# Performance work log

Hardware: AMD Instinct MI355X
Metric: run time of the kernel (lower is better)

## Reference

```python
import jax, jax.numpy as jnp
import numpy as np

H = 768   # hidden_size
E = 9     # num_entity_types
R = 10    # num_relation_types
B, S, N = 8, 4096, 64
P = N * (N - 1) // 2  # 2016 ordered pairs i<j


def setup_inputs() -> dict:
    key = jax.random.key(0)
    ks = jax.random.split(key, 10)
    sd = 0.02
    return {
        "sequence_output": jax.random.normal(ks[0], (B, S, H), jnp.float32),
        "attention_mask": jnp.ones((B, S), jnp.int32),
        "entity_spans": jnp.sort(jax.random.randint(ks[1], (B, N, 2), 0, S), axis=-1),
        # entity_classifier: Linear(H, H//2) -> ReLU -> Linear(H//2, E)
        "w1": jax.random.normal(ks[2], (H, H // 2), jnp.float32) * sd,
        "b1": jnp.zeros((H // 2,), jnp.float32),
        "w2": jax.random.normal(ks[3], (H // 2, E), jnp.float32) * sd,
        "b2": jnp.zeros((E,), jnp.float32),
        # relation_classifier: Linear(2H, H) -> ReLU -> Linear(H, R)
        "rw1": jax.random.normal(ks[4], (2 * H, H), jnp.float32) * sd,
        "rb1": jnp.zeros((H,), jnp.float32),
        "rw2": jax.random.normal(ks[5], (H, R), jnp.float32) * sd,
        "rb2": jnp.zeros((R,), jnp.float32),
    }


def reference(sequence_output, attention_mask, entity_spans,
              w1, b1, w2, b2, rw1, rb1, rw2, rb2):
    # entity classifier over all tokens (dropout is identity in eval)
    h = jax.nn.relu(jnp.einsum('bsh,hf->bsf', sequence_output, w1) + b1)
    entity_logits = jnp.einsum('bsf,fe->bse', h, w2) + b2  # [B,S,E]

    # span mean-pooling via a [B,N,S] membership mask (segment-mean)
    pos = jnp.arange(S)
    start = entity_spans[..., 0:1]  # [B,N,1]
    end = entity_spans[..., 1:2]    # [B,N,1]
    mask = ((pos >= start) & (pos < end)).astype(sequence_output.dtype)  # [B,N,S]
    counts = jnp.clip(mask.sum(-1, keepdims=True), 1.0)  # avoid /0 for empty spans
    entity_reprs = jnp.einsum('bns,bsh->bnh', mask, sequence_output) / counts  # [B,N,H]
    pooled_logits = jnp.einsum('bns,bse->bne', mask, entity_logits) / counts   # [B,N,E]
    entity_types = jnp.argmax(pooled_logits, axis=-1)  # [B,N]

    # all i<j pairs, batched relation classifier (replaces per-pair Python loop)
    ii, jj = np.triu_indices(N, k=1)  # static index sets, len P
    pair = jnp.concatenate([entity_reprs[:, ii], entity_reprs[:, jj]], axis=-1)  # [B,P,2H]
    rh = jax.nn.relu(jnp.einsum('bpk,kh->bph', pair, rw1) + rb1)
    relation_logits = jnp.einsum('bph,hr->bpr', rh, rw2) + rb2  # [B,P,R]
    relation_types = jnp.argmax(relation_logits, axis=-1)  # [B,P]

    return entity_logits, relation_logits, entity_reprs, entity_types, relation_types
```

## Files before the change

### kernel.cpp

```cpp
#include <hip/hip_runtime.h>
#include <hip/hip_bf16.h>

#define Hh 768
#define Ff 384
#define Ee 9
#define Rr 10
#define Bb 8
#define Ss 4096
#define Nn_ENT 64
#define Pp 2016
#define CH 16
#define NC 256

typedef short bf16x8 __attribute__((ext_vector_type(8)));
typedef float f32x4 __attribute__((ext_vector_type(4)));

__device__ __forceinline__ void async_copy16(void* lds, const void* g) {
  auto* l = (__attribute__((address_space(3))) unsigned int*)(lds);
  auto* p = (const __attribute__((address_space(1))) unsigned int*)(g);
  __builtin_amdgcn_global_load_lds(p, l, 16, 0, 0);
}

__global__ __launch_bounds__(256) void transpose_w1(const float* __restrict__ w1,
                                                    unsigned short* __restrict__ wt) {
  __shared__ unsigned short tile[64][65];
  const int bk = blockIdx.x * 64;
  const int bc = blockIdx.y * 64;
  const int c = threadIdx.x & 63, kq = threadIdx.x >> 6;
#pragma unroll
  for (int i = 0; i < 16; ++i) {
    int k = kq * 16 + i;
    float v = w1[(size_t)(bk + k) * Ff + bc + c];
    tile[c][k] = __bfloat16_as_ushort(__float2bfloat16(v));
  }
  __syncthreads();
  const int k2 = threadIdx.x & 63, cq = threadIdx.x >> 6;
#pragma unroll
  for (int i = 0; i < 16; ++i) {
    int c2 = cq * 16 + i;
    wt[(size_t)(bc + c2) * Hh + bk + k2] = tile[c2][k2];
  }
}

__global__ __launch_bounds__(512, 4) void gemm1_fused(const float* __restrict__ A,
                                                      const unsigned short* __restrict__ Wt,
                                                      const float* __restrict__ b1,
                                                      const float* __restrict__ w2,
                                                      const float* __restrict__ b2,
                                                      float* __restrict__ elog,
                                                      float* __restrict__ Pc) {
  __shared__ float As[64 * 64];
  __shared__ unsigned short Bs[384 * 64];
  __shared__ float w2s[Ff * Ee];
  __shared__ float b1s[Ff];
  __shared__ float b2s[Ee];
  float* red = (float*)&Bs[0];

  const int t = threadIdx.x;
  const int wid = t >> 6, lane = t & 63;
  const int wm = wid >> 2, wn = wid & 3;
  const int fr = lane & 15, fq = lane >> 4;
  const int row0 = blockIdx.x * 64;
  const int bb = row0 >> 12;
  const int c0 = (row0 & (Ss - 1)) >> 4;

  for (int i = t; i < Ff * Ee; i += 512) w2s[i] = w2[i];
  for (int i = t; i < Ff; i += 512) b1s[i] = b1[i];
  if (t < Ee) b2s[t] = b2[t];

  const int brow0 = (lane >> 3);
  const int bgr = lane & 7;

  f32x4 acc[2][6] = {};
  const int sB = (fr & 7);

#pragma unroll 1
  for (int ks = 0; ks < Hh / 64; ++ks) {
    const int k0 = ks * 64;
#pragma unroll
    for (int i = 0; i < 2; ++i) {
      const int rl = (wid * 2 + i) * 4 + (lane >> 4);
      const int g = (lane & 15) ^ (rl & 15);
      async_copy16(&As[(wid * 2 + i) * 256],
                   A + (size_t)(row0 + rl) * Hh + k0 + g * 4);
    }
#pragma unroll
    for (int j = 0; j < 6; ++j) {
      const int e = wid * 6 + j;
      const int rl = e * 8 + brow0;
      const int g = bgr ^ (rl & 7);
      async_copy16(&Bs[e * 512],
                   Wt + (size_t)rl * Hh + k0 + g * 8);
    }
    __syncthreads();

#pragma unroll
    for (int kk = 0; kk < 2; ++kk) {
      bf16x8 af[2], bfr[6];
#pragma unroll
      for (int m = 0; m < 2; ++m) {
        const int R = wm * 32 + m * 16 + fr;
        const int G0 = 2 * (kk * 4 + fq);
        const float* rowp = &As[R * 64];
        float4 v0 = *(const float4*)(rowp + ((G0 ^ fr) * 4));
        float4 v1 = *(const float4*)(rowp + (((G0 + 1) ^ fr) * 4));
        union { bf16x8 v; __hip_bfloat162 h2[4]; } u;
        u.h2[0] = __float22bfloat162_rn(float2{v0.x, v0.y});
        u.h2[1] = __float22bfloat162_rn(float2{v0.z, v0.w});
        u.h2[2] = __float22bfloat162_rn(float2{v1.x, v1.y});
        u.h2[3] = __float22bfloat162_rn(float2{v1.z, v1.w});
        af[m] = u.v;
      }
      const int gB = ((kk * 4 + fq) ^ sB) * 8;
#pragma unroll
      for (int n = 0; n < 6; ++n)
        bfr[n] = *(const bf16x8*)&Bs[(wn * 96 + n * 16 + fr) * 64 + gB];
#pragma unroll
      for (int m = 0; m < 2; ++m)
#pragma unroll
        for (int n = 0; n < 6; ++n)
          acc[m][n] = __builtin_amdgcn_mfma_f32_16x16x32_bf16(af[m], bfr[n], acc[m][n], 0, 0, 0);
    }

    if (t < 256) {
      const int cc = t >> 6, kq = lane & 15, rh = lane >> 4;
      float4 s = {0.f, 0.f, 0.f, 0.f};
#pragma unroll
      for (int q = 0; q < 4; ++q) {
        const int row = cc * 16 + rh * 4 + q;
        const int slot = kq ^ (rh * 4 + q);
        float4 v = *(const float4*)&As[row * 64 + slot * 4];
        s.x += v.x; s.y += v.y; s.z += v.z; s.w += v.w;
      }
      s.x += __shfl_xor(s.x, 16); s.y += __shfl_xor(s.y, 16);
      s.z += __shfl_xor(s.z, 16); s.w += __shfl_xor(s.w, 16);
      s.x += __shfl_xor(s.x, 32); s.y += __shfl_xor(s.y, 32);
      s.z += __shfl_xor(s.z, 32); s.w += __shfl_xor(s.w, 32);
      if (rh == 0)
        *(float4*)&Pc[((size_t)(bb * NC + c0 + cc)) * Hh + k0 + kq * 4] = s;
    }
    __syncthreads();
  }

#pragma unroll
  for (int m = 0; m < 2; ++m) {
#pragma unroll
    for (int j = 0; j < 4; ++j) {
      float p[Ee];
#pragma unroll
      for (int e = 0; e < Ee; ++e) p[e] = 0.f;
#pragma unroll
      for (int n = 0; n < 6; ++n) {
        const int col = wn * 96 + n * 16 + fr;
        const float hv = fmaxf(acc[m][n][j] + b1s[col], 0.f);
        const float* wrow = &w2s[col * Ee];
#pragma unroll
        for (int e = 0; e < Ee; ++e) p[e] = fmaf(hv, wrow[e], p[e]);
      }
#pragma unroll
      for (int mask = 1; mask <= 8; mask <<= 1)
#pragma unroll
        for (int e = 0; e < Ee; ++e) p[e] += __shfl_xor(p[e], mask);
      if (fr < Ee) {
        const int row = wm * 32 + m * 16 + fq * 4 + j;
        red[(wn * 64 + row) * Ee + fr] = p[fr];
      }
    }
  }
  __syncthreads();
  for (int idx = t; idx < 64 * Ee; idx += 512) {
    const int row = idx / Ee, e = idx - row * Ee;
    float v = red[(0 * 64 + row) * Ee + e] + red[(1 * 64 + row) * Ee + e]
            + red[(2 * 64 + row) * Ee + e] + red[(3 * 64 + row) * Ee + e] + b2s[e];
    elog[(size_t)(row0 + row) * Ee + e] = v;
  }
}

__global__ __launch_bounds__(256) void gemm_uv_splitk(const float* __restrict__ A,
                                                      const float* __restrict__ rw1,
                                                      float* __restrict__ part) {
  const int uv = blockIdx.z & 1, ks = blockIdx.z >> 1;
  const float* Wp = rw1 + (size_t)uv * Hh * Hh + (size_t)ks * 192 * Hh;
  __shared__ float Ast[16][68];
  __shared__ float Wst[16][68];
  const int t = threadIdx.x;
  const int row0 = blockIdx.x * 64, col0 = blockIdx.y * 64;
  const int tm = (t & 15) * 4, tn = (t >> 4) * 4;
  const int lr = t >> 2, lk = (t & 3) * 4;
  const int wk = t >> 4, wc = (t & 15) * 4;
  float acc[4][4] = {};
  const float* Arow = A + (size_t)(row0 + lr) * Hh + ks * 192 + lk;
  for (int k0 = 0; k0 < 192; k0 += 16) {
    float4 av = *(const float4*)(Arow + k0);
    Ast[lk + 0][lr] = av.x; Ast[lk + 1][lr] = av.y;
    Ast[lk + 2][lr] = av.z; Ast[lk + 3][lr] = av.w;
    *(float4*)&Wst[wk][wc] = *(const float4*)(Wp + (size_t)(k0 + wk) * Hh + col0 + wc);
    __syncthreads();
#pragma unroll
    for (int kk = 0; kk < 16; ++kk) {
      const float4 a = *(const float4*)&Ast[kk][tm];
      const float4 b = *(const float4*)&Wst[kk][tn];
      acc[0][0] = fmaf(a.x, b.x, acc[0][0]); acc[0][1] = fmaf(a.x, b.y, acc[0][1]);
      acc[0][2] = fmaf(a.x, b.z, acc[0][2]); acc[0][3] = fmaf(a.x, b.w, acc[0][3]);
      acc[1][0] = fmaf(a.y, b.x, acc[1][0]); acc[1][1] = fmaf(a.y, b.y, acc[1][1]);
      acc[1][2] = fmaf(a.y, b.z, acc[1][2]); acc[1][3] = fmaf(a.y, b.w, acc[1][3]);
      acc[2][0] = fmaf(a.z, b.x, acc[2][0]); acc[2][1] = fmaf(a.z, b.y, acc[2][1]);
      acc[2][2] = fmaf(a.z, b.z, acc[2][2]); acc[2][3] = fmaf(a.z, b.w, acc[2][3]);
      acc[3][0] = fmaf(a.w, b.x, acc[3][0]); acc[3][1] = fmaf(a.w, b.y, acc[3][1]);
      acc[3][2] = fmaf(a.w, b.z, acc[3][2]); acc[3][3] = fmaf(a.w, b.w, acc[3][3]);
    }
    __syncthreads();
  }
  float* out = part + ((size_t)ks * 2 + uv) * (512 * Hh);
#pragma unroll
  for (int i = 0; i < 4; ++i) {
    float4 o; o.x = acc[i][0]; o.y = acc[i][1]; o.z = acc[i][2]; o.w = acc[i][3];
    *(float4*)(out + (size_t)(row0 + tm + i) * Hh + col0 + tn) = o;
  }
}

__global__ __launch_bounds__(256) void uv_reduce(const float* __restrict__ part,
                                                 float* __restrict__ uv) {
  const int i = blockIdx.x * 256 + threadIdx.x;
  const float4* p = (const float4*)part;
  float4 a = p[i], b = p[i + 196608], c = p[i + 2 * 196608], d = p[i + 3 * 196608];
  float4 o;
  o.x = (a.x + b.x) + (c.x + d.x);
  o.y = (a.y + b.y) + (c.y + d.y);
  o.z = (a.z + b.z) + (c.z + d.z);
  o.w = (a.w + b.w) + (c.w + d.w);
  ((float4*)uv)[i] = o;
}

__global__ __launch_bounds__(256) void chunk_scan(float* __restrict__ Pc) {
  __shared__ float tile[NC][64];
  const int b = blockIdx.y;
  const int h0 = blockIdx.x * 64;
  float* base = Pc + (size_t)b * NC * Hh + h0;
  const int l = threadIdx.x & 63, g = threadIdx.x >> 6;
#pragma unroll 4
  for (int c = g * 64; c < g * 64 + 64; ++c)
    tile[c][l] = base[(size_t)c * Hh + l];
  __syncthreads();
  float run = 0.f;
#pragma unroll 4
  for (int c = g * 64; c < g * 64 + 64; ++c) {
    run += tile[c][l];
    tile[c][l] = run;
  }
  __syncthreads();
  float off = 0.f;
#pragma unroll
  for (int gg = 0; gg < 3; ++gg)
    if (gg < g) off += tile[gg * 64 + 63][l];
  __syncthreads();
  if (g > 0) {
#pragma unroll 4
    for (int c = g * 64; c < g * 64 + 64; ++c)
      tile[c][l] += off;
  }
  __syncthreads();
#pragma unroll 4
  for (int c = g * 64; c < g * 64 + 64; ++c)
    base[(size_t)c * Hh + l] = tile[c][l];
}

__global__ __launch_bounds__(192) void entity_reprs_k(const float* __restrict__ seq,
                                                      const float* __restrict__ Pc,
                                                      const int* __restrict__ spans,
                                                      float* __restrict__ reprs) {
  const int bn = blockIdx.x;
  const int b = bn >> 6;
  const int start = spans[bn * 2], end = spans[bn * 2 + 1];
  const int cnt = max(end - start, 1);
  const float inv = 1.0f / (float)cnt;
  const int cs = (start + CH - 1) >> 4, ce = end >> 4;
  const float* seqb = seq + (size_t)b * Ss * Hh;
  const float4* Pcb = (const float4*)(Pc + (size_t)b * NC * Hh);
  const int t = threadIdx.x;
  float4 acc = {0.f, 0.f, 0.f, 0.f};
  if (cs <= ce) {
    if (cs < ce) {
      float4 hi = Pcb[(size_t)(ce - 1) * 192 + t];
      acc.x += hi.x; acc.y += hi.y; acc.z += hi.z; acc.w += hi.w;
      if (cs > 0) {
        float4 lo = Pcb[(size_t)(cs - 1) * 192 + t];
        acc.x -= lo.x; acc.y -= lo.y; acc.z -= lo.z; acc.w -= lo.w;
      }
    }
    for (int s = start; s < cs * CH; ++s) {
      float4 v = ((const float4*)(seqb + (size_t)s * Hh))[t];
      acc.x += v.x; acc.y += v.y; acc.z += v.z; acc.w += v.w;
    }
    for (int s = ce * CH; s < end; ++s) {
      float4 v = ((const float4*)(seqb + (size_t)s * Hh))[t];
      acc.x += v.x; acc.y += v.y; acc.z += v.z; acc.w += v.w;
    }
  } else {
    for (int s = start; s < end; ++s) {
      float4 v = ((const float4*)(seqb + (size_t)s * Hh))[t];
      acc.x += v.x; acc.y += v.y; acc.z += v.z; acc.w += v.w;
    }
  }
  float4 o; o.x = acc.x * inv; o.y = acc.y * inv; o.z = acc.z * inv; o.w = acc.w * inv;
  ((float4*)(reprs + (size_t)bn * Hh))[t] = o;
}

__global__ __launch_bounds__(256) void pooled_argmax(const float* __restrict__ elog,
                                                     const int* __restrict__ spans,
                                                     float* __restrict__ etypes) {
  __shared__ float red[4][Ee];
  const int bn = blockIdx.x;
  const int b = bn >> 6;
  const int start = spans[bn * 2], end = spans[bn * 2 + 1];
  const int t = threadIdx.x, lane = t & 63, w = t >> 6;
  float acc[Ee];
#pragma unroll
  for (int e = 0; e < Ee; ++e) acc[e] = 0.f;
  const float* p = elog + (size_t)b * Ss * Ee;
  for (int s = start + t; s < end; s += 256) {
    const float* q = p + (size_t)s * Ee;
#pragma unroll
    for (int e = 0; e < Ee; ++e) acc[e] += q[e];
  }
#pragma unroll
  for (int off = 32; off; off >>= 1)
#pragma unroll
    for (int e = 0; e < Ee; ++e) acc[e] += __shfl_down(acc[e], off);
  if (lane == 0) {
#pragma unroll
    for (int e = 0; e < Ee; ++e) red[w][e] = acc[e];
  }
  __syncthreads();
  if (t == 0) {
    int best = 0; float bv = -1e30f;
#pragma unroll
    for (int e = 0; e < Ee; ++e) {
      float v = red[0][e] + red[1][e] + red[2][e] + red[3][e];
      if (v > bv) { bv = v; best = e; }
    }
    etypes[bn] = (float)best;
  }
}

__global__ __launch_bounds__(256) void relations_k(const float* __restrict__ UV,
                                                   const float* __restrict__ rb1,
                                                   const float* __restrict__ rw2,
                                                   const float* __restrict__ rb2,
                                                   float* __restrict__ rlogits,
                                                   float* __restrict__ rtypes) {
  __shared__ float w2l[Hh * 11];
  __shared__ float b1l[Hh];
  const int t = threadIdx.x;
  for (int i = t; i < Hh * Rr; i += 256) {
    const int k = i / Rr, r = i - k * Rr;
    w2l[k * 11 + r] = rw2[i];
  }
  for (int i = t; i < Hh; i += 256) b1l[i] = rb1[i];
  __syncthreads();

  const int p = blockIdx.x * 4 + (t >> 6);
  const int lane = t & 63;
  const int b = p / Pp, pp = p % Pp;
  int i = 0, off = 0;
  while (off + (Nn_ENT - 1 - i) <= pp) { off += Nn_ENT - 1 - i; ++i; }
  const int j = i + 1 + (pp - off);
  const float* u = UV + ((size_t)b * Nn_ENT + i) * Hh;
  const float* v = UV + (size_t)512 * Hh + ((size_t)b * Nn_ENT + j) * Hh;
  float acc[Rr];
#pragma unroll
  for (int r = 0; r < Rr; ++r) acc[r] = 0.f;
  for (int k = lane; k < Hh; k += 64) {
    float x = fmaxf(u[k] + v[k] + b1l[k], 0.f);
    const float* w = &w2l[k * 11];
#pragma unroll
    for (int r = 0; r < Rr; ++r) acc[r] = fmaf(x, w[r], acc[r]);
  }
#pragma unroll
  for (int off2 = 32; off2; off2 >>= 1)
#pragma unroll
    for (int r = 0; r < Rr; ++r) acc[r] += __shfl_down(acc[r], off2);
  if (lane == 0) {
    int best = 0; float bv = acc[0] + rb2[0];
    rlogits[(size_t)p * Rr + 0] = bv;
#pragma unroll
    for (int r = 1; r < Rr; ++r) {
      float val = acc[r] + rb2[r];
      rlogits[(size_t)p * Rr + r] = val;
      if (val > bv) { bv = val; best = r; }
    }
    rtypes[p] = (float)best;
  }
}

extern "C" void kernel_launch(void* const* d_in, const int* in_sizes, int n_in,
                              void* d_out, int out_size, void* d_ws, size_t ws_size,
                              hipStream_t stream) {
  const float* seq   = (const float*)d_in[0];
  const int*   spans = (const int*)d_in[2];
  const float* w1    = (const float*)d_in[3];
  const float* b1    = (const float*)d_in[4];
  const float* w2    = (const float*)d_in[5];
  const float* b2    = (const float*)d_in[6];
  const float* rw1   = (const float*)d_in[7];
  const float* rb1   = (const float*)d_in[8];
  const float* rw2   = (const float*)d_in[9];
  const float* rb2   = (const float*)d_in[10];

  float* out_elog = (float*)d_out;
  float* out_rlog = out_elog + 294912;
  float* out_repr = out_rlog + 161280;
  float* out_etyp = out_repr + 393216;
  float* out_rtyp = out_etyp + 512;

  float*          ws_pc  = (float*)d_ws;
  float*          ws_uv  = (float*)((char*)d_ws + 6291456);
  unsigned short* ws_wt  = (unsigned short*)((char*)d_ws + 9437184);
  float*          ws_uvp = (float*)((char*)d_ws + 10027008);

  transpose_w1<<<dim3(12, 6), 256, 0, stream>>>(w1, ws_wt);
  gemm1_fused<<<512, 512, 0, stream>>>(seq, ws_wt, b1, w2, b2, out_elog, ws_pc);
  chunk_scan<<<dim3(Hh / 64, Bb), 256, 0, stream>>>(ws_pc);
  entity_reprs_k<<<512, 192, 0, stream>>>(seq, ws_pc, spans, out_repr);
  gemm_uv_splitk<<<dim3(8, 12, 8), 256, 0, stream>>>(out_repr, rw1, ws_uvp);
  uv_reduce<<<768, 256, 0, stream>>>(ws_uvp, ws_uv);
  pooled_argmax<<<512, 256, 0, stream>>>(out_elog, spans, out_etyp);
  relations_k<<<4032, 256, 0, stream>>>(ws_uv, rb1, rw2, rb2, out_rlog, out_rtyp);
}
```

Before: 147.1 us.

## Split gemm1 hidden dimension across two workgroups with partial-logit reduction kernel

The fused entity GEMM now splits the 384-wide hidden dimension into two 192-column halves, doubling the grid to 1024 workgroups with a swizzled block-index mapping, and halves per-block LDS and accumulators. Each half writes partial entity logits to workspace, and a new elog_reduce kernel sums them and adds b2. The aim is more blocks and occupancy for 256 CUs. The cost is that the fp32 A tile is loaded and converted twice, plus an extra launch and a partial-buffer round trip.

```diff
diff --git a/kernel.cpp b/kernel.cpp
--- a/kernel.cpp
+++ b/kernel.cpp
@@ -46,32 +46,33 @@
                                                       const unsigned short* __restrict__ Wt,
                                                       const float* __restrict__ b1,
                                                       const float* __restrict__ w2,
-                                                      const float* __restrict__ b2,
-                                                      float* __restrict__ elog,
+                                                      float* __restrict__ epart,
                                                       float* __restrict__ Pc) {
   __shared__ float As[64 * 64];
-  __shared__ unsigned short Bs[384 * 64];
-  __shared__ float w2s[Ff * Ee];
-  __shared__ float b1s[Ff];
-  __shared__ float b2s[Ee];
+  __shared__ unsigned short Bs[192 * 64];
+  __shared__ float w2s[192 * Ee];
+  __shared__ float b1s[192];
   float* red = (float*)&Bs[0];
 
   const int t = threadIdx.x;
   const int wid = t >> 6, lane = t & 63;
-  const int wm = wid >> 2, wn = wid & 3;
+  const int wm = wid >> 1, wn = wid & 1;
   const int fr = lane & 15, fq = lane >> 4;
-  const int row0 = blockIdx.x * 64;
+  const int wg = blockIdx.x;
+  const int lin = (wg & 7) * 128 + (wg >> 3);
+  const int mt = lin >> 1, nt = lin & 1;
+  const int row0 = mt * 64;
+  const int col0 = nt * 192;
   const int bb = row0 >> 12;
   const int c0 = (row0 & (Ss - 1)) >> 4;
 
-  for (int i = t; i < Ff * Ee; i += 512) w2s[i] = w2[i];
-  for (int i = t; i < Ff; i += 512) b1s[i] = b1[i];
-  if (t < Ee) b2s[t] = b2[t];
+  for (int i = t; i < 192 * Ee; i += 512) w2s[i] = w2[(size_t)col0 * Ee + i];
+  for (int i = t; i < 192; i += 512) b1s[i] = b1[col0 + i];
 
   const int brow0 = (lane >> 3);
   const int bgr = lane & 7;
 
-  f32x4 acc[2][6] = {};
+  f32x4 acc[6] = {};
   const int sB = (fr & 7);
 
 #pragma unroll 1
@@ -85,21 +86,20 @@
                    A + (size_t)(row0 + rl) * Hh + k0 + g * 4);
     }
 #pragma unroll
-    for (int j = 0; j < 6; ++j) {
-      const int e = wid * 6 + j;
+    for (int j = 0; j < 3; ++j) {
+      const int e = wid * 3 + j;
       const int rl = e * 8 + brow0;
       const int g = bgr ^ (rl & 7);
       async_copy16(&Bs[e * 512],
-                   Wt + (size_t)rl * Hh + k0 + g * 8);
+                   Wt + (size_t)(col0 + rl) * Hh + k0 + g * 8);
     }
     __syncthreads();
 
 #pragma unroll
     for (int kk = 0; kk < 2; ++kk) {
-      bf16x8 af[2], bfr[6];
-#pragma unroll
-      for (int m = 0; m < 2; ++m) {
-        const int R = wm * 32 + m * 16 + fr;
+      bf16x8 af, bfr[6];
+      {
+        const int R = wm * 16 + fr;
         const int G0 = 2 * (kk * 4 + fq);
         const float* rowp = &As[R * 64];
         float4 v0 = *(const float4*)(rowp + ((G0 ^ fr) * 4));
@@ -109,26 +109,24 @@
         u.h2[1] = __float22bfloat162_rn(float2{v0.z, v0.w});
         u.h2[2] = __float22bfloat162_rn(float2{v1.x, v1.y});
         u.h2[3] = __float22bfloat162_rn(float2{v1.z, v1.w});
-        af[m] = u.v;
+        af = u.v;
       }
       const int gB = ((kk * 4 + fq) ^ sB) * 8;
 #pragma unroll
       for (int n = 0; n < 6; ++n)
         bfr[n] = *(const bf16x8*)&Bs[(wn * 96 + n * 16 + fr) * 64 + gB];
 #pragma unroll
-      for (int m = 0; m < 2; ++m)
-#pragma unroll
-        for (int n = 0; n < 6; ++n)
-          acc[m][n] = __builtin_amdgcn_mfma_f32_16x16x32_bf16(af[m], bfr[n], acc[m][n], 0, 0, 0);
-    }
-
-    if (t < 256) {
-      const int cc = t >> 6, kq = lane & 15, rh = lane >> 4;
+      for (int n = 0; n < 6; ++n)
+        acc[n] = __builtin_amdgcn_mfma_f32_16x16x32_bf16(af, bfr[n], acc[n], 0, 0, 0);
+    }
+
+    if (nt == 0 && t < 256) {
+      const int cc = t >> 6, kq2 = lane & 15, rh = lane >> 4;
       float4 s = {0.f, 0.f, 0.f, 0.f};
 #pragma unroll
       for (int q = 0; q < 4; ++q) {
         const int row = cc * 16 + rh * 4 + q;
-        const int slot = kq ^ (rh * 4 + q);
+        const int slot = kq2 ^ (rh * 4 + q);
         float4 v = *(const float4*)&As[row * 64 + slot * 4];
         s.x += v.x; s.y += v.y; s.z += v.z; s.w += v.w;
       }
@@ -137,43 +135,46 @@
       s.x += __shfl_xor(s.x, 32); s.y += __shfl_xor(s.y, 32);
       s.z += __shfl_xor(s.z, 32); s.w += __shfl_xor(s.w, 32);
       if (rh == 0)
-        *(float4*)&Pc[((size_t)(bb * NC + c0 + cc)) * Hh + k0 + kq * 4] = s;
+        *(float4*)&Pc[((size_t)(bb * NC + c0 + cc)) * Hh + k0 + kq2 * 4] = s;
     }
     __syncthreads();
   }
 
 #pragma unroll
-  for (int m = 0; m < 2; ++m) {
-#pragma unroll
-    for (int j = 0; j < 4; ++j) {
-      float p[Ee];
-#pragma unroll
-      for (int e = 0; e < Ee; ++e) p[e] = 0.f;
-#pragma unroll
-      for (int n = 0; n < 6; ++n) {
-        const int col = wn * 96 + n * 16 + fr;
-        const float hv = fmaxf(acc[m][n][j] + b1s[col], 0.f);
-        const float* wrow = &w2s[col * Ee];
-#pragma unroll
-        for (int e = 0; e < Ee; ++e) p[e] = fmaf(hv, wrow[e], p[e]);
-      }
-#pragma unroll
-      for (int mask = 1; mask <= 8; mask <<= 1)
-#pragma unroll
-        for (int e = 0; e < Ee; ++e) p[e] += __shfl_xor(p[e], mask);
-      if (fr < Ee) {
-        const int row = wm * 32 + m * 16 + fq * 4 + j;
-        red[(wn * 64 + row) * Ee + fr] = p[fr];
-      }
+  for (int j = 0; j < 4; ++j) {
+    float p[Ee];
+#pragma unroll
+    for (int e = 0; e < Ee; ++e) p[e] = 0.f;
+#pragma unroll
+    for (int n = 0; n < 6; ++n) {
+      const int cl = wn * 96 + n * 16 + fr;
+      const float hv = fmaxf(acc[n][j] + b1s[cl], 0.f);
+      const float* wrow = &w2s[cl * Ee];
+#pragma unroll
+      for (int e = 0; e < Ee; ++e) p[e] = fmaf(hv, wrow[e], p[e]);
+    }
+#pragma unroll
+    for (int mask = 1; mask <= 8; mask <<= 1)
+#pragma unroll
+      for (int e = 0; e < Ee; ++e) p[e] += __shfl_xor(p[e], mask);
+    if (fr < Ee) {
+      const int row = wm * 16 + fq * 4 + j;
+      red[(wn * 64 + row) * Ee + fr] = p[fr];
     }
   }
   __syncthreads();
   for (int idx = t; idx < 64 * Ee; idx += 512) {
     const int row = idx / Ee, e = idx - row * Ee;
-    float v = red[(0 * 64 + row) * Ee + e] + red[(1 * 64 + row) * Ee + e]
-            + red[(2 * 64 + row) * Ee + e] + red[(3 * 64 + row) * Ee + e] + b2s[e];
-    elog[(size_t)(row0 + row) * Ee + e] = v;
-  }
+    float v = red[row * Ee + e] + red[(64 + row) * Ee + e];
+    epart[(size_t)nt * (32768 * Ee) + (size_t)(row0 + row) * Ee + e] = v;
+  }
+}
+
+__global__ __launch_bounds__(256) void elog_reduce(const float* __restrict__ epart,
+                                                   const float* __restrict__ b2,
+                                                   float* __restrict__ elog) {
+  const int idx = blockIdx.x * 256 + threadIdx.x;
+  elog[idx] = epart[idx] + epart[idx + 294912] + b2[idx % Ee];
 }
 
 __global__ __launch_bounds__(256) void gemm_uv_splitk(const float* __restrict__ A,
@@ -417,9 +418,11 @@
   float*          ws_uv  = (float*)((char*)d_ws + 6291456);
   unsigned short* ws_wt  = (unsigned short*)((char*)d_ws + 9437184);
   float*          ws_uvp = (float*)((char*)d_ws + 10027008);
+  float*          ws_ep  = (float*)((char*)d_ws + 22609920);
 
   transpose_w1<<<dim3(12, 6), 256, 0, stream>>>(w1, ws_wt);
-  gemm1_fused<<<512, 512, 0, stream>>>(seq, ws_wt, b1, w2, b2, out_elog, ws_pc);
+  gemm1_fused<<<1024, 512, 0, stream>>>(seq, ws_wt, b1, w2, ws_ep, ws_pc);
+  elog_reduce<<<1152, 256, 0, stream>>>(ws_ep, b2, out_elog);
   chunk_scan<<<dim3(Hh / 64, Bb), 256, 0, stream>>>(ws_pc);
   entity_reprs_k<<<512, 192, 0, stream>>>(seq, ws_pc, spans, out_repr);
   gemm_uv_splitk<<<dim3(8, 12, 8), 256, 0, stream>>>(out_repr, rw1, ws_uvp);
```

Measured after the change: 156.4 us. +6.3%, slower.
